# Optimization experiments

Hardware: AMD Instinct MI355X
Metric: run time of the kernel (lower is better)

Reference implementation:

```python
import jax, jax.numpy as jnp
import numpy as np
from jax.ops import segment_sum, segment_max

N, E, G = 20000, 100000, 16
TILE, EMB, HID, OUT, FEAT, HEADS = 32, 128, 256, 512, 512, 8
SLOPE = 0.2


def setup_inputs() -> dict:
    key = jax.random.key(0)
    ks = jax.random.split(key, 20)
    def gn(k, shape, fan_in):
        return jax.random.normal(k, shape, jnp.float32) * (1.0 / np.sqrt(fan_in))
    return {
        "x": jax.random.normal(ks[0], (N, TILE), jnp.float32),
        "edge_index": jax.random.randint(ks[1], (2, E), 0, N, jnp.int32),
        "batch": jnp.sort(jax.random.randint(ks[2], (N,), 0, G, jnp.int32)),
        "W0": gn(ks[3], (TILE, EMB), TILE), "b0": jnp.zeros((EMB,), jnp.float32),
        "W1": gn(ks[4], (EMB, HEADS * HID), EMB),
        "a1s": gn(ks[5], (HEADS, HID), HID), "a1d": gn(ks[6], (HEADS, HID), HID),
        "b1": jnp.zeros((HEADS * HID,), jnp.float32),
        "W2": gn(ks[7], (HEADS * HID, HEADS * HID), HEADS * HID),
        "a2s": gn(ks[8], (HEADS, HID), HID), "a2d": gn(ks[9], (HEADS, HID), HID),
        "b2": jnp.zeros((HEADS * HID,), jnp.float32),
        "W3": gn(ks[10], (HEADS * HID, OUT), HEADS * HID),
        "a3s": gn(ks[11], (1, OUT), OUT), "a3d": gn(ks[12], (1, OUT), OUT),
        "b3": jnp.zeros((OUT,), jnp.float32),
        "Wf": gn(ks[13], (OUT, FEAT), OUT), "bf": jnp.zeros((FEAT,), jnp.float32),
    }


def gat_conv(x, src, dst, W, a_s, a_d, b, heads, ch, n):
    # PyG GATConv: linear, per-edge additive attention, segment softmax over dst, scatter-add
    h = (x @ W).reshape(n, heads, ch)                       # [N,H,C]
    e_src = jnp.einsum("nhc,hc->nh", h, a_s)                 # [N,H]
    e_dst = jnp.einsum("nhc,hc->nh", h, a_d)
    e = jax.nn.leaky_relu(e_src[src] + e_dst[dst], SLOPE)    # [E,H]
    m = segment_max(e, dst, num_segments=n)                  # [N,H]
    m = jax.lax.stop_gradient(jnp.where(jnp.isfinite(m), m, 0.0))
    ex = jnp.exp(e - m[dst])
    den = segment_sum(ex, dst, num_segments=n)
    alpha = ex / (den[dst] + 1e-16)                          # [E,H]
    out = segment_sum(h[src] * alpha[..., None], dst, num_segments=n)  # [N,H,C]
    return out.reshape(n, heads * ch) + b


def reference(x, edge_index, batch, W0, b0, W1, a1s, a1d, b1, W2, a2s, a2d, b2,
              W3, a3s, a3d, b3, Wf, bf):
    loop = jnp.arange(N, dtype=edge_index.dtype)             # PyG adds self-loops by default
    src = jnp.concatenate([edge_index[0], loop])
    dst = jnp.concatenate([edge_index[1], loop])
    h = jax.nn.leaky_relu(x @ W0 + b0, SLOPE)
    h = jax.nn.leaky_relu(gat_conv(h, src, dst, W1, a1s, a1d, b1, HEADS, HID, N), SLOPE)
    h = jax.nn.leaky_relu(gat_conv(h, src, dst, W2, a2s, a2d, b2, HEADS, HID, N), SLOPE)
    h = jax.nn.leaky_relu(gat_conv(h, src, dst, W3, a3s, a3d, b3, 1, OUT, N), SLOPE)
    sums = segment_sum(h, batch, num_segments=G)             # global_mean_pool
    cnt = segment_sum(jnp.ones((N,), h.dtype), batch, num_segments=G)
    mean = sums / jnp.maximum(cnt, 1.0)[:, None]
    return jax.nn.leaky_relu(mean @ Wf + bf, SLOPE)
```

## Files before the change

kernel.cpp:

```cpp
#include <hip/hip_runtime.h>
#include <hip/hip_bf16.h>

#define N_NODES 20000
#define N_EDGES 100000
#define ET (N_EDGES + N_NODES)
#define G_GRAPHS 16
#define SLOPE 0.2f

using short8  = __attribute__((ext_vector_type(8))) short;
using floatx4 = __attribute__((ext_vector_type(4))) float;

__device__ __forceinline__ float lrelu(float x) { return x > 0.f ? x : SLOPE * x; }

__device__ __forceinline__ float b2f(unsigned short u) {
    union { unsigned int i; float f; } v; v.i = ((unsigned int)u) << 16; return v.f;
}
__device__ __forceinline__ unsigned short f2b(float f) {
    union { float f; unsigned int i; } v; v.f = f;
    unsigned int i = v.i;
    return (unsigned short)((i + 0x7fffu + ((i >> 16) & 1u)) >> 16);
}

__device__ __forceinline__ void atomicMaxF(float* addr, float val) {
    if (val >= 0.f) atomicMax((int*)addr, __float_as_int(val));
    else            atomicMin((unsigned int*)addr, (unsigned int)__float_as_int(val));
}

__device__ __forceinline__ void gld16(const void* g, void* l) {
    __builtin_amdgcn_global_load_lds((const __attribute__((address_space(1))) void*)g,
                                     (__attribute__((address_space(3))) void*)l, 16, 0, 0);
}

__device__ int dev_lower_bound(const int* a, int n, int key) {
    int lo = 0, hi = n;
    while (lo < hi) { int mid = (lo + hi) >> 1; if (a[mid] < key) lo = mid + 1; else hi = mid; }
    return lo;
}

__global__ void zero_kernel(int* __restrict__ p, int n) {
    int i = blockIdx.x * blockDim.x + threadIdx.x;
    if (i < n) p[i] = 0;
}
__global__ void fillf_kernel(float* __restrict__ p, int n, float v) {
    int i = blockIdx.x * blockDim.x + threadIdx.x;
    if (i < n) p[i] = v;
}

__global__ void count_kernel(const int* __restrict__ ei, int* __restrict__ counts) {
    int e = blockIdx.x * blockDim.x + threadIdx.x;
    if (e >= ET) return;
    int dst = (e < N_EDGES) ? ei[N_EDGES + e] : (e - N_EDGES);
    atomicAdd(&counts[dst], 1);
}

__global__ void scan_kernel(const int* __restrict__ counts, int* __restrict__ row_ptr) {
    __shared__ int sums[256];
    int t = threadIdx.x;
    const int CH = (N_NODES + 255) / 256;
    int base = t * CH;
    int s = 0;
    for (int i = 0; i < CH; i++) { int idx = base + i; if (idx < N_NODES) s += counts[idx]; }
    sums[t] = s;
    __syncthreads();
    for (int off = 1; off < 256; off <<= 1) {
        int v = (t >= off) ? sums[t - off] : 0;
        __syncthreads();
        sums[t] += v;
        __syncthreads();
    }
    int run = (t == 0) ? 0 : sums[t - 1];
    for (int i = 0; i < CH; i++) {
        int idx = base + i;
        if (idx < N_NODES) { row_ptr[idx] = run; run += counts[idx]; }
    }
    if (t == 255) row_ptr[N_NODES] = run;
}

__global__ void fill_kernel(const int* __restrict__ ei, const int* __restrict__ row_ptr,
                            int* __restrict__ fill_cnt, int* __restrict__ col) {
    int e = blockIdx.x * blockDim.x + threadIdx.x;
    if (e >= ET) return;
    int src, dst;
    if (e < N_EDGES) { src = ei[e]; dst = ei[N_EDGES + e]; }
    else             { src = dst = e - N_EDGES; }
    int pos = atomicAdd(&fill_cnt[dst], 1);
    col[row_ptr[dst] + pos] = src;
}

__global__ void transpose_kernel(const float* __restrict__ W, unsigned short* __restrict__ Wt,
                                 int K, int N) {
    __shared__ float tile[32][33];
    int bn = blockIdx.x * 32, bk = blockIdx.y * 32;
    int tx = threadIdx.x & 31, ty = threadIdx.x >> 5;
#pragma unroll
    for (int p = 0; p < 32; p += 8)
        tile[ty + p][tx] = W[(size_t)(bk + ty + p) * N + bn + tx];
    __syncthreads();
#pragma unroll
    for (int p = 0; p < 32; p += 8)
        Wt[(size_t)(bn + ty + p) * K + bk + tx] = f2b(tile[tx][ty + p]);
}

__global__ void gemm0_kernel(const float* __restrict__ x, const float* __restrict__ W0,
                             const float* __restrict__ b0, unsigned short* __restrict__ h0) {
    __shared__ float xr[32];
    int n = blockIdx.x, t = threadIdx.x;
    if (t < 32) xr[t] = x[n * 32 + t];
    __syncthreads();
    float acc = 0.f;
#pragma unroll
    for (int k = 0; k < 32; k++) acc += xr[k] * W0[k * 128 + t];
    h0[(size_t)n * 128 + t] = f2b(lrelu(acc + b0[t]));
}

__global__ __launch_bounds__(256) void gemm_mfma(const unsigned short* __restrict__ A,
                                                 const unsigned short* __restrict__ Bt,
                                                 unsigned short* __restrict__ C,
                                                 int M, int N, int K) {
    __shared__ __align__(16) unsigned short As[128][32];
    __shared__ __align__(16) unsigned short Bs[128][32];
    int t = threadIdx.x;
    int w = t >> 6, l = t & 63;
    int r0 = blockIdx.y * 128, c0 = blockIdx.x * 128;
    int wr = (w >> 1) * 64, wc = (w & 1) * 64;
    int lrow = l >> 2, lcol = (l & 3) * 8;
    int m16 = l & 15, q8 = (l >> 4) * 8;
    floatx4 acc[4][4] = {};

    for (int k0 = 0; k0 < K; k0 += 32) {
        __syncthreads();
#pragma unroll
        for (int q = 0; q < 2; q++) {
            int row = w * 32 + q * 16 + lrow;
            int ga = min(r0 + row, M - 1);
            gld16(A + (size_t)ga * K + k0 + lcol, &As[w * 32 + q * 16][0]);
            gld16(Bt + (size_t)(c0 + row) * K + k0 + lcol, &Bs[w * 32 + q * 16][0]);
        }
        __syncthreads();
        short8 af[4], bfr[4];
#pragma unroll
        for (int i = 0; i < 4; i++) af[i] = *(const short8*)&As[wr + i * 16 + m16][q8];
#pragma unroll
        for (int j = 0; j < 4; j++) bfr[j] = *(const short8*)&Bs[wc + j * 16 + m16][q8];
#pragma unroll
        for (int i = 0; i < 4; i++)
#pragma unroll
            for (int j = 0; j < 4; j++)
                acc[i][j] = __builtin_amdgcn_mfma_f32_16x16x32_bf16(af[i], bfr[j], acc[i][j], 0, 0, 0);
    }
    int quad = l >> 4;
#pragma unroll
    for (int i = 0; i < 4; i++)
#pragma unroll
        for (int j = 0; j < 4; j++)
#pragma unroll
            for (int reg = 0; reg < 4; reg++) {
                int r = r0 + wr + i * 16 + quad * 4 + reg;
                int c = c0 + wc + j * 16 + m16;
                if (r < M) C[(size_t)r * N + c] = f2b(acc[i][j][reg]);
            }
}

__global__ void att8_kernel(const unsigned short* __restrict__ h, const float* __restrict__ a_s,
                            const float* __restrict__ a_d, float* __restrict__ es,
                            float* __restrict__ ed) {
    int n = blockIdx.x, t = threadIdx.x;
    int hd = t >> 5, l = t & 31;
    const unsigned short* hr = h + (size_t)n * 2048 + hd * 256 + l * 8;
    const float* as_ = a_s + hd * 256 + l * 8;
    const float* ad_ = a_d + hd * 256 + l * 8;
    uint4 u = *(const uint4*)hr;
    float v[8] = { b2f((unsigned short)(u.x & 0xffff)), b2f((unsigned short)(u.x >> 16)),
                   b2f((unsigned short)(u.y & 0xffff)), b2f((unsigned short)(u.y >> 16)),
                   b2f((unsigned short)(u.z & 0xffff)), b2f((unsigned short)(u.z >> 16)),
                   b2f((unsigned short)(u.w & 0xffff)), b2f((unsigned short)(u.w >> 16)) };
    float s1 = 0.f, s2 = 0.f;
#pragma unroll
    for (int j = 0; j < 8; j++) { s1 += v[j] * as_[j]; s2 += v[j] * ad_[j]; }
    for (int m = 16; m >= 1; m >>= 1) { s1 += __shfl_xor(s1, m); s2 += __shfl_xor(s2, m); }
    if (l == 0) { es[n * 8 + hd] = s1; ed[n * 8 + hd] = s2; }
}

__global__ void att1_kernel(const unsigned short* __restrict__ h, const float* __restrict__ a_s,
                            const float* __restrict__ a_d, float* __restrict__ es,
                            float* __restrict__ ed) {
    int n = blockIdx.x, l = threadIdx.x;
    const unsigned short* hr = h + (size_t)n * 512 + l * 8;
    const float* as_ = a_s + l * 8;
    const float* ad_ = a_d + l * 8;
    uint4 u = *(const uint4*)hr;
    float v[8] = { b2f((unsigned short)(u.x & 0xffff)), b2f((unsigned short)(u.x >> 16)),
                   b2f((unsigned short)(u.y & 0xffff)), b2f((unsigned short)(u.y >> 16)),
                   b2f((unsigned short)(u.z & 0xffff)), b2f((unsigned short)(u.z >> 16)),
                   b2f((unsigned short)(u.w & 0xffff)), b2f((unsigned short)(u.w >> 16)) };
    float s1 = 0.f, s2 = 0.f;
#pragma unroll
    for (int j = 0; j < 8; j++) { s1 += v[j] * as_[j]; s2 += v[j] * ad_[j]; }
    for (int m = 32; m >= 1; m >>= 1) { s1 += __shfl_xor(s1, m); s2 += __shfl_xor(s2, m); }
    if (l == 0) { es[n] = s1; ed[n] = s2; }
}

template <int H>
__global__ void edge_max_kernel(const int* __restrict__ ei, const float* __restrict__ es,
                                const float* __restrict__ ed, float* __restrict__ mx) {
    int idx = blockIdx.x * blockDim.x + threadIdx.x;
    if (idx >= ET * H) return;
    int e = idx / H, h = idx % H;
    int src, dst;
    if (e < N_EDGES) { src = ei[e]; dst = ei[N_EDGES + e]; }
    else             { src = dst = e - N_EDGES; }
    float lg = lrelu(es[src * H + h] + ed[dst * H + h]);
    atomicMaxF(&mx[dst * H + h], lg);
}

template <int H>
__global__ void edge_sum_kernel(const int* __restrict__ ei, const float* __restrict__ es,
                                const float* __restrict__ ed, const float* __restrict__ mx,
                                float* __restrict__ den) {
    int idx = blockIdx.x * blockDim.x + threadIdx.x;
    if (idx >= ET * H) return;
    int e = idx / H, h = idx % H;
    int src, dst;
    if (e < N_EDGES) { src = ei[e]; dst = ei[N_EDGES + e]; }
    else             { src = dst = e - N_EDGES; }
    float lg = lrelu(es[src * H + h] + ed[dst * H + h]);
    atomicAdd(&den[dst * H + h], __expf(lg - mx[dst * H + h]));
}

template <int H, int C>
__global__ __launch_bounds__(256) void agg_kernel(const unsigned short* __restrict__ hmid,
                                                  const float* __restrict__ es,
                                                  const float* __restrict__ ed,
                                                  const float* __restrict__ mx,
                                                  const float* __restrict__ den,
                                                  const int* __restrict__ row_ptr,
                                                  const int* __restrict__ col,
                                                  const float* __restrict__ bias,
                                                  unsigned short* __restrict__ out) {
    constexpr int HC = H * C;
    constexpr int PT = HC / 256;
    __shared__ float sm_alpha[32][H];
    __shared__ float sm_m[H], sm_den[H], sm_ed[H];
    __shared__ int scol[32];
    int v = blockIdx.x, t = threadIdx.x;
    int rs = row_ptr[v], deg = row_ptr[v + 1] - rs;
    if (t < H) { sm_m[t] = mx[v * H + t]; sm_den[t] = den[v * H + t]; sm_ed[t] = ed[v * H + t]; }
    int j0 = t * PT;
    int hd = j0 / C;
    float acc[PT] = {};
    for (int cs = 0; cs < deg; cs += 32) {
        int cn = min(32, deg - cs);
        __syncthreads();
        if (t < cn) scol[t] = col[rs + cs + t];
        __syncthreads();
        if (t < cn * H) {
            int ce = t / H, hh = t % H;
            float lg = lrelu(es[scol[ce] * H + hh] + sm_ed[hh]);
            sm_alpha[ce][hh] = __expf(lg - sm_m[hh]) / (sm_den[hh] + 1e-16f);
        }
        __syncthreads();
        for (int ce = 0; ce < cn; ce++) {
            float a = sm_alpha[ce][hd];
            const unsigned short* hr = hmid + (size_t)scol[ce] * HC + j0;
            if constexpr (PT == 8) {
                uint4 u = *(const uint4*)hr;
                acc[0] += a * b2f((unsigned short)(u.x & 0xffff));
                acc[1] += a * b2f((unsigned short)(u.x >> 16));
                acc[2] += a * b2f((unsigned short)(u.y & 0xffff));
                acc[3] += a * b2f((unsigned short)(u.y >> 16));
                acc[4] += a * b2f((unsigned short)(u.z & 0xffff));
                acc[5] += a * b2f((unsigned short)(u.z >> 16));
                acc[6] += a * b2f((unsigned short)(u.w & 0xffff));
                acc[7] += a * b2f((unsigned short)(u.w >> 16));
            } else {
                unsigned int u = *(const unsigned int*)hr;
                acc[0] += a * b2f((unsigned short)(u & 0xffff));
                acc[1] += a * b2f((unsigned short)(u >> 16));
            }
        }
    }
    unsigned short o[PT];
#pragma unroll
    for (int i = 0; i < PT; i++) o[i] = f2b(lrelu(acc[i] + bias[j0 + i]));
    if constexpr (PT == 8) {
        *(uint4*)&out[(size_t)v * HC + j0] = *(const uint4*)o;
    } else {
        *(unsigned int*)&out[(size_t)v * HC + j0] = *(const unsigned int*)o;
    }
}

__global__ void pool_kernel(const unsigned short* __restrict__ h3, const int* __restrict__ batch,
                            float* __restrict__ msum) {
    int b0 = blockIdx.x * 128, t = threadIdx.x;
    int nend = min(b0 + 128, N_NODES);
    int curg = batch[b0];
    float s0 = 0.f, s1 = 0.f;
    for (int n = b0; n < nend; n++) {
        int g = batch[n];
        if (g != curg) {
            atomicAdd(&msum[curg * 512 + t * 2], s0);
            atomicAdd(&msum[curg * 512 + t * 2 + 1], s1);
            s0 = s1 = 0.f; curg = g;
        }
        unsigned int u = *(const unsigned int*)&h3[(size_t)n * 512 + t * 2];
        s0 += b2f((unsigned short)(u & 0xffff));
        s1 += b2f((unsigned short)(u >> 16));
    }
    atomicAdd(&msum[curg * 512 + t * 2], s0);
    atomicAdd(&msum[curg * 512 + t * 2 + 1], s1);
}

__global__ void final_kernel(const float* __restrict__ msum, const int* __restrict__ batch,
                             const float* __restrict__ Wf, const float* __restrict__ bf,
                             float* __restrict__ out) {
    int g = blockIdx.x, t = threadIdx.x;
    __shared__ float mr[512];
    __shared__ float sinv;
    if (t == 0) {
        int st = dev_lower_bound(batch, N_NODES, g);
        int en = dev_lower_bound(batch, N_NODES, g + 1);
        sinv = 1.f / fmaxf((float)(en - st), 1.f);
    }
    __syncthreads();
    for (int c = t; c < 512; c += 256) mr[c] = msum[g * 512 + c] * sinv;
    __syncthreads();
    for (int j = t; j < 512; j += 256) {
        float s = 0.f;
        for (int k = 0; k < 512; k++) s += mr[k] * Wf[k * 512 + j];
        out[g * 512 + j] = lrelu(s + bf[j]);
    }
}

extern "C" void kernel_launch(void* const* d_in, const int* in_sizes, int n_in,
                              void* d_out, int out_size, void* d_ws, size_t ws_size,
                              hipStream_t stream) {
    const float* x   = (const float*)d_in[0];
    const int*   ei  = (const int*)d_in[1];
    const int*   bat = (const int*)d_in[2];
    const float* W0  = (const float*)d_in[3];
    const float* b0  = (const float*)d_in[4];
    const float* W1  = (const float*)d_in[5];
    const float* a1s = (const float*)d_in[6];
    const float* a1d = (const float*)d_in[7];
    const float* b1  = (const float*)d_in[8];
    const float* W2  = (const float*)d_in[9];
    const float* a2s = (const float*)d_in[10];
    const float* a2d = (const float*)d_in[11];
    const float* b2  = (const float*)d_in[12];
    const float* W3  = (const float*)d_in[13];
    const float* a3s = (const float*)d_in[14];
    const float* a3d = (const float*)d_in[15];
    const float* b3  = (const float*)d_in[16];
    const float* Wf  = (const float*)d_in[17];
    const float* bf  = (const float*)d_in[18];
    float* out = (float*)d_out;

    char* p = (char*)d_ws;
    unsigned short* bufA = (unsigned short*)p; p += (size_t)N_NODES * 2048 * 2;
    unsigned short* bufB = (unsigned short*)p; p += (size_t)N_NODES * 2048 * 2;
    unsigned short* h0   = (unsigned short*)p; p += (size_t)N_NODES * 128 * 2;
    unsigned short* W1t  = (unsigned short*)p; p += (size_t)2048 * 128 * 2;
    unsigned short* W2t  = (unsigned short*)p; p += (size_t)2048 * 2048 * 2;
    unsigned short* W3t  = (unsigned short*)p; p += (size_t)512 * 2048 * 2;
    float* es   = (float*)p; p += (size_t)N_NODES * 8 * 4;
    float* ed   = (float*)p; p += (size_t)N_NODES * 8 * 4;
    float* mx   = (float*)p; p += (size_t)N_NODES * 8 * 4;
    float* den  = (float*)p; p += (size_t)N_NODES * 8 * 4;
    float* msum = (float*)p; p += 16 * 512 * 4;
    int* counts  = (int*)p; p += (size_t)N_NODES * 4;
    int* row_ptr = (int*)p; p += (size_t)(N_NODES + 1) * 4;
    int* col     = (int*)p; p += (size_t)ET * 4;

    zero_kernel<<<(N_NODES + 255) / 256, 256, 0, stream>>>(counts, N_NODES);
    count_kernel<<<(ET + 255) / 256, 256, 0, stream>>>(ei, counts);
    scan_kernel<<<1, 256, 0, stream>>>(counts, row_ptr);
    zero_kernel<<<(N_NODES + 255) / 256, 256, 0, stream>>>(counts, N_NODES);
    fill_kernel<<<(ET + 255) / 256, 256, 0, stream>>>(ei, row_ptr, counts, col);

    transpose_kernel<<<dim3(2048 / 32, 128 / 32), 256, 0, stream>>>(W1, W1t, 128, 2048);
    transpose_kernel<<<dim3(2048 / 32, 2048 / 32), 256, 0, stream>>>(W2, W2t, 2048, 2048);
    transpose_kernel<<<dim3(512 / 32, 2048 / 32), 256, 0, stream>>>(W3, W3t, 2048, 512);

    gemm0_kernel<<<N_NODES, 128, 0, stream>>>(x, W0, b0, h0);

    dim3 g12(2048 / 128, (N_NODES + 127) / 128);
    dim3 g3(512 / 128, (N_NODES + 127) / 128);
    int eb8 = (ET * 8 + 255) / 256, eb1 = (ET + 255) / 256;

    gemm_mfma<<<g12, 256, 0, stream>>>(h0, W1t, bufB, N_NODES, 2048, 128);
    att8_kernel<<<N_NODES, 256, 0, stream>>>(bufB, a1s, a1d, es, ed);
    fillf_kernel<<<(N_NODES * 8 + 255) / 256, 256, 0, stream>>>(mx, N_NODES * 8, -1e30f);
    fillf_kernel<<<(N_NODES * 8 + 255) / 256, 256, 0, stream>>>(den, N_NODES * 8, 0.f);
    edge_max_kernel<8><<<eb8, 256, 0, stream>>>(ei, es, ed, mx);
    edge_sum_kernel<8><<<eb8, 256, 0, stream>>>(ei, es, ed, mx, den);
    agg_kernel<8, 256><<<N_NODES, 256, 0, stream>>>(bufB, es, ed, mx, den, row_ptr, col, b1, bufA);

    gemm_mfma<<<g12, 256, 0, stream>>>(bufA, W2t, bufB, N_NODES, 2048, 2048);
    att8_kernel<<<N_NODES, 256, 0, stream>>>(bufB, a2s, a2d, es, ed);
    fillf_kernel<<<(N_NODES * 8 + 255) / 256, 256, 0, stream>>>(mx, N_NODES * 8, -1e30f);
    fillf_kernel<<<(N_NODES * 8 + 255) / 256, 256, 0, stream>>>(den, N_NODES * 8, 0.f);
    edge_max_kernel<8><<<eb8, 256, 0, stream>>>(ei, es, ed, mx);
    edge_sum_kernel<8><<<eb8, 256, 0, stream>>>(ei, es, ed, mx, den);
    agg_kernel<8, 256><<<N_NODES, 256, 0, stream>>>(bufB, es, ed, mx, den, row_ptr, col, b2, bufA);

    gemm_mfma<<<g3, 256, 0, stream>>>(bufA, W3t, bufB, N_NODES, 512, 2048);
    att1_kernel<<<N_NODES, 64, 0, stream>>>(bufB, a3s, a3d, es, ed);
    fillf_kernel<<<(N_NODES + 255) / 256, 256, 0, stream>>>(mx, N_NODES, -1e30f);
    fillf_kernel<<<(N_NODES + 255) / 256, 256, 0, stream>>>(den, N_NODES, 0.f);
    edge_max_kernel<1><<<eb1, 256, 0, stream>>>(ei, es, ed, mx);
    edge_sum_kernel<1><<<eb1, 256, 0, stream>>>(ei, es, ed, mx, den);
    agg_kernel<1, 512><<<N_NODES, 256, 0, stream>>>(bufB, es, ed, mx, den, row_ptr, col, b3, bufA);

    zero_kernel<<<(16 * 512 + 255) / 256, 256, 0, stream>>>((int*)msum, 16 * 512);
    pool_kernel<<<(N_NODES + 127) / 128, 256, 0, stream>>>(bufA, bat, msum);
    final_kernel<<<G_GRAPHS, 256, 0, stream>>>(msum, bat, Wf, bf, out);
}
```

Measured before the change: 884.6 us.

## Fuse segment softmax into CSR aggregation and swizzle GEMM LDS layout

Removes the separate atomic edge-max and edge-sum kernels and their fill kernels. Each destination node's block now computes the softmax max and denominator itself by walking its CSR neighbor list with block reductions before aggregating. This drops global atomics and several launches per layer, at the cost of reading the neighbor logits three times per block. Separately, the MFMA GEMM applies an XOR swizzle to LDS column chunks to reduce bank conflicts on fragment reads.

```diff
diff --git a/kernel.cpp b/kernel.cpp
--- a/kernel.cpp
+++ b/kernel.cpp
@@ -21,11 +21,6 @@
     return (unsigned short)((i + 0x7fffu + ((i >> 16) & 1u)) >> 16);
 }
 
-__device__ __forceinline__ void atomicMaxF(float* addr, float val) {
-    if (val >= 0.f) atomicMax((int*)addr, __float_as_int(val));
-    else            atomicMin((unsigned int*)addr, (unsigned int)__float_as_int(val));
-}
-
 __device__ __forceinline__ void gld16(const void* g, void* l) {
     __builtin_amdgcn_global_load_lds((const __attribute__((address_space(1))) void*)g,
                                      (__attribute__((address_space(3))) void*)l, 16, 0, 0);
@@ -40,10 +35,6 @@
 __global__ void zero_kernel(int* __restrict__ p, int n) {
     int i = blockIdx.x * blockDim.x + threadIdx.x;
     if (i < n) p[i] = 0;
-}
-__global__ void fillf_kernel(float* __restrict__ p, int n, float v) {
-    int i = blockIdx.x * blockDim.x + threadIdx.x;
-    if (i < n) p[i] = v;
 }
 
 __global__ void count_kernel(const int* __restrict__ ei, int* __restrict__ counts) {
@@ -123,8 +114,11 @@
     int w = t >> 6, l = t & 63;
     int r0 = blockIdx.y * 128, c0 = blockIdx.x * 128;
     int wr = (w >> 1) * 64, wc = (w & 1) * 64;
-    int lrow = l >> 2, lcol = (l & 3) * 8;
-    int m16 = l & 15, q8 = (l >> 4) * 8;
+    int lrow = l >> 2;
+    int gcb  = (l & 3) ^ ((l >> 3) & 3);
+    int m16 = l & 15, qb = l >> 4;
+    int sw  = (m16 >> 1) & 3;
+    int roff = ((qb ^ sw) * 8);
     floatx4 acc[4][4] = {};
 
     for (int k0 = 0; k0 < K; k0 += 32) {
@@ -133,15 +127,15 @@
         for (int q = 0; q < 2; q++) {
             int row = w * 32 + q * 16 + lrow;
             int ga = min(r0 + row, M - 1);
-            gld16(A + (size_t)ga * K + k0 + lcol, &As[w * 32 + q * 16][0]);
-            gld16(Bt + (size_t)(c0 + row) * K + k0 + lcol, &Bs[w * 32 + q * 16][0]);
+            gld16(A + (size_t)ga * K + k0 + gcb * 8, &As[w * 32 + q * 16][0]);
+            gld16(Bt + (size_t)(c0 + row) * K + k0 + gcb * 8, &Bs[w * 32 + q * 16][0]);
         }
         __syncthreads();
         short8 af[4], bfr[4];
 #pragma unroll
-        for (int i = 0; i < 4; i++) af[i] = *(const short8*)&As[wr + i * 16 + m16][q8];
-#pragma unroll
-        for (int j = 0; j < 4; j++) bfr[j] = *(const short8*)&Bs[wc + j * 16 + m16][q8];
+        for (int i = 0; i < 4; i++) af[i] = *(const short8*)&As[wr + i * 16 + m16][roff];
+#pragma unroll
+        for (int j = 0; j < 4; j++) bfr[j] = *(const short8*)&Bs[wc + j * 16 + m16][roff];
 #pragma unroll
         for (int i = 0; i < 4; i++)
 #pragma unroll
@@ -200,51 +194,51 @@
     if (l == 0) { es[n] = s1; ed[n] = s2; }
 }
 
-template <int H>
-__global__ void edge_max_kernel(const int* __restrict__ ei, const float* __restrict__ es,
-                                const float* __restrict__ ed, float* __restrict__ mx) {
-    int idx = blockIdx.x * blockDim.x + threadIdx.x;
-    if (idx >= ET * H) return;
-    int e = idx / H, h = idx % H;
-    int src, dst;
-    if (e < N_EDGES) { src = ei[e]; dst = ei[N_EDGES + e]; }
-    else             { src = dst = e - N_EDGES; }
-    float lg = lrelu(es[src * H + h] + ed[dst * H + h]);
-    atomicMaxF(&mx[dst * H + h], lg);
-}
-
-template <int H>
-__global__ void edge_sum_kernel(const int* __restrict__ ei, const float* __restrict__ es,
-                                const float* __restrict__ ed, const float* __restrict__ mx,
-                                float* __restrict__ den) {
-    int idx = blockIdx.x * blockDim.x + threadIdx.x;
-    if (idx >= ET * H) return;
-    int e = idx / H, h = idx % H;
-    int src, dst;
-    if (e < N_EDGES) { src = ei[e]; dst = ei[N_EDGES + e]; }
-    else             { src = dst = e - N_EDGES; }
-    float lg = lrelu(es[src * H + h] + ed[dst * H + h]);
-    atomicAdd(&den[dst * H + h], __expf(lg - mx[dst * H + h]));
-}
-
 template <int H, int C>
-__global__ __launch_bounds__(256) void agg_kernel(const unsigned short* __restrict__ hmid,
-                                                  const float* __restrict__ es,
-                                                  const float* __restrict__ ed,
-                                                  const float* __restrict__ mx,
-                                                  const float* __restrict__ den,
-                                                  const int* __restrict__ row_ptr,
-                                                  const int* __restrict__ col,
-                                                  const float* __restrict__ bias,
-                                                  unsigned short* __restrict__ out) {
+__global__ __launch_bounds__(256) void agg_fused(const unsigned short* __restrict__ hmid,
+                                                 const float* __restrict__ es,
+                                                 const float* __restrict__ ed,
+                                                 const int* __restrict__ row_ptr,
+                                                 const int* __restrict__ col,
+                                                 const float* __restrict__ bias,
+                                                 unsigned short* __restrict__ out) {
     constexpr int HC = H * C;
     constexpr int PT = HC / 256;
+    constexpr int LH = (H == 8) ? 3 : 0;
+    __shared__ float sm_ed[H], sm_m[H], sm_den[H];
+    __shared__ float wpart[4 * H];
     __shared__ float sm_alpha[32][H];
-    __shared__ float sm_m[H], sm_den[H], sm_ed[H];
     __shared__ int scol[32];
     int v = blockIdx.x, t = threadIdx.x;
     int rs = row_ptr[v], deg = row_ptr[v + 1] - rs;
-    if (t < H) { sm_m[t] = mx[v * H + t]; sm_den[t] = den[v * H + t]; sm_ed[t] = ed[v * H + t]; }
+    if (t < H) sm_ed[t] = ed[v * H + t];
+    __syncthreads();
+    int h = t & (H - 1);
+    int w = t >> 6, l = t & 63;
+    float edv = sm_ed[h];
+    float lmax = -1e30f;
+    for (int e = t >> LH; e < deg; e += 256 / H) {
+        int s = col[rs + e];
+        lmax = fmaxf(lmax, lrelu(es[s * H + h] + edv));
+    }
+#pragma unroll
+    for (int m = H; m < 64; m <<= 1) lmax = fmaxf(lmax, __shfl_xor(lmax, m));
+    if (l < H) wpart[w * H + l] = lmax;
+    __syncthreads();
+    if (t < H)
+        sm_m[t] = fmaxf(fmaxf(wpart[t], wpart[H + t]), fmaxf(wpart[2 * H + t], wpart[3 * H + t]));
+    __syncthreads();
+    float mh = sm_m[h];
+    float lsum = 0.f;
+    for (int e = t >> LH; e < deg; e += 256 / H) {
+        int s = col[rs + e];
+        lsum += __expf(lrelu(es[s * H + h] + edv) - mh);
+    }
+#pragma unroll
+    for (int m = H; m < 64; m <<= 1) lsum += __shfl_xor(lsum, m);
+    if (l < H) wpart[w * H + l] = lsum;
+    __syncthreads();
+    if (t < H) sm_den[t] = wpart[t] + wpart[H + t] + wpart[2 * H + t] + wpart[3 * H + t];
     int j0 = t * PT;
     int hd = j0 / C;
     float acc[PT] = {};
@@ -364,8 +358,6 @@
     unsigned short* W3t  = (unsigned short*)p; p += (size_t)512 * 2048 * 2;
     float* es   = (float*)p; p += (size_t)N_NODES * 8 * 4;
     float* ed   = (float*)p; p += (size_t)N_NODES * 8 * 4;
-    float* mx   = (float*)p; p += (size_t)N_NODES * 8 * 4;
-    float* den  = (float*)p; p += (size_t)N_NODES * 8 * 4;
     float* msum = (float*)p; p += 16 * 512 * 4;
     int* counts  = (int*)p; p += (size_t)N_NODES * 4;
     int* row_ptr = (int*)p; p += (size_t)(N_NODES + 1) * 4;
@@ -385,31 +377,18 @@
 
     dim3 g12(2048 / 128, (N_NODES + 127) / 128);
     dim3 g3(512 / 128, (N_NODES + 127) / 128);
-    int eb8 = (ET * 8 + 255) / 256, eb1 = (ET + 255) / 256;
 
     gemm_mfma<<<g12, 256, 0, stream>>>(h0, W1t, bufB, N_NODES, 2048, 128);
     att8_kernel<<<N_NODES, 256, 0, stream>>>(bufB, a1s, a1d, es, ed);
-    fillf_kernel<<<(N_NODES * 8 + 255) / 256, 256, 0, stream>>>(mx, N_NODES * 8, -1e30f);
-    fillf_kernel<<<(N_NODES * 8 + 255) / 256, 256, 0, stream>>>(den, N_NODES * 8, 0.f);
-    edge_max_kernel<8><<<eb8, 256, 0, stream>>>(ei, es, ed, mx);
-    edge_sum_kernel<8><<<eb8, 256, 0, stream>>>(ei, es, ed, mx, den);
-    agg_kernel<8, 256><<<N_NODES, 256, 0, stream>>>(bufB, es, ed, mx, den, row_ptr, col, b1, bufA);
+    agg_fused<8, 256><<<N_NODES, 256, 0, stream>>>(bufB, es, ed, row_ptr, col, b1, bufA);
 
     gemm_mfma<<<g12, 256, 0, stream>>>(bufA, W2t, bufB, N_NODES, 2048, 2048);
     att8_kernel<<<N_NODES, 256, 0, stream>>>(bufB, a2s, a2d, es, ed);
-    fillf_kernel<<<(N_NODES * 8 + 255) / 256, 256, 0, stream>>>(mx, N_NODES * 8, -1e30f);
-    fillf_kernel<<<(N_NODES * 8 + 255) / 256, 256, 0, stream>>>(den, N_NODES * 8, 0.f);
-    edge_max_kernel<8><<<eb8, 256, 0, stream>>>(ei, es, ed, mx);
-    edge_sum_kernel<8><<<eb8, 256, 0, stream>>>(ei, es, ed, mx, den);
-    agg_kernel<8, 256><<<N_NODES, 256, 0, stream>>>(bufB, es, ed, mx, den, row_ptr, col, b2, bufA);
+    agg_fused<8, 256><<<N_NODES, 256, 0, stream>>>(bufB, es, ed, row_ptr, col, b2, bufA);
 
     gemm_mfma<<<g3, 256, 0, stream>>>(bufA, W3t, bufB, N_NODES, 512, 2048);
     att1_kernel<<<N_NODES, 64, 0, stream>>>(bufB, a3s, a3d, es, ed);
-    fillf_kernel<<<(N_NODES + 255) / 256, 256, 0, stream>>>(mx, N_NODES, -1e30f);
-    fillf_kernel<<<(N_NODES + 255) / 256, 256, 0, stream>>>(den, N_NODES, 0.f);
-    edge_max_kernel<1><<<eb1, 256, 0, stream>>>(ei, es, ed, mx);
-    edge_sum_kernel<1><<<eb1, 256, 0, stream>>>(ei, es, ed, mx, den);
-    agg_kernel<1, 512><<<N_NODES, 256, 0, stream>>>(bufB, es, ed, mx, den, row_ptr, col, b3, bufA);
+    agg_fused<1, 512><<<N_NODES, 256, 0, stream>>>(bufB, es, ed, row_ptr, col, b3, bufA);
 
     zero_kernel<<<(16 * 512 + 255) / 256, 256, 0, stream>>>((int*)msum, 16 * 512);
     pool_kernel<<<(N_NODES + 127) / 128, 256, 0, stream>>>(bufA, bat, msum);
```

Result: faster. 836.4 us (-5.4%).
